# Kernel tuning notes

Measured on AMD Instinct MI355X. Metric: run time of the kernel, lower is better.

Reference implementation:

```python
import jax, jax.numpy as jnp
import numpy as np

B, L, D_MODEL = 4, 2048, 1024
N_HEADS, FEAT, HEAD_DIM = 16, 16, 64
CHUNK = 128
EPS = 1e-12


def taylor_exp(x):
    """2nd-order Taylor feature map of exp(q.k/sqrt(d)).
    x: (b, h, l, f) -> (b, h, l, 1 + f + f*f)"""
    f = x.shape[-1]
    r2 = jnp.sqrt(jnp.asarray(2.0, x.dtype))
    rd = jnp.sqrt(jnp.asarray(float(f), x.dtype))      # sqrt(d)
    rrd = jnp.sqrt(rd)                                  # d**0.25
    x2 = (x[..., :, None] * x[..., None, :]).reshape(*x.shape[:-1], f * f) / r2
    ones = jnp.ones_like(x[..., :1])
    return jnp.concatenate([ones, x / rrd, x2 / rd], axis=-1)


def setup_inputs() -> dict:
    key = jax.random.key(0)
    k1, k2, k3, k4, k5 = jax.random.split(key, 5)
    s = 0.02
    return {
        "hidden_states": jax.random.normal(k1, (B, L, D_MODEL), jnp.float32),
        "Wq": jax.random.normal(k2, (N_HEADS * FEAT, D_MODEL), jnp.float32) * s,
        "Wk": jax.random.normal(k3, (N_HEADS * FEAT, D_MODEL), jnp.float32) * s,
        "Wv": jax.random.normal(k4, (N_HEADS * HEAD_DIM, D_MODEL), jnp.float32) * s,
        "Wo": jax.random.normal(k5, (D_MODEL, N_HEADS * HEAD_DIM), jnp.float32) * s,
    }


def reference(hidden_states, Wq, Wk, Wv, Wo):
    b, l, _ = hidden_states.shape
    # projections (Linear without bias: x @ W.T)
    q = (hidden_states @ Wq.T).reshape(b, l, N_HEADS, FEAT).transpose(0, 2, 1, 3)
    k = (hidden_states @ Wk.T).reshape(b, l, N_HEADS, FEAT).transpose(0, 2, 1, 3)
    v = (hidden_states @ Wv.T).reshape(b, l, N_HEADS, HEAD_DIM).transpose(0, 2, 1, 3)

    qf = taylor_exp(q)  # (b, h, l, De) with De = 1 + f + f^2 = 273
    kf = taylor_exp(k)
    De = qf.shape[-1]

    # chunked causal linear attention: same math as cumulative kv-state
    n = l // CHUNK
    qc = jnp.moveaxis(qf.reshape(b, N_HEADS, n, CHUNK, De), 2, 0)       # (n,b,h,c,De)
    kc = jnp.moveaxis(kf.reshape(b, N_HEADS, n, CHUNK, De), 2, 0)
    vc = jnp.moveaxis(v.reshape(b, N_HEADS, n, CHUNK, HEAD_DIM), 2, 0)
    mask = jnp.tril(jnp.ones((CHUNK, CHUNK), qf.dtype))

    def step(carry, xs):
        S, z = carry                       # S: (b,h,De,e), z: (b,h,De)
        qi, ki, vi = xs
        attn = jnp.einsum('bhid,bhjd->bhij', qi, ki) * mask
        num = jnp.einsum('bhij,bhje->bhie', attn, vi) \
            + jnp.einsum('bhid,bhde->bhie', qi, S)
        den = attn.sum(-1) + jnp.einsum('bhid,bhd->bhi', qi, z)
        yi = num / (den[..., None] + EPS)
        S = S + jnp.einsum('bhjd,bhje->bhde', ki, vi)
        z = z + ki.sum(2)
        return (S, z), yi

    S0 = jnp.zeros((b, N_HEADS, De, HEAD_DIM), qf.dtype)
    z0 = jnp.zeros((b, N_HEADS, De), qf.dtype)
    _, ys = jax.lax.scan(step, (S0, z0), (qc, kc, vc))
    y = jnp.moveaxis(ys, 0, 2).reshape(b, N_HEADS, l, HEAD_DIM)          # (b,h,l,e)
    y = y.transpose(0, 2, 1, 3).reshape(b, l, N_HEADS * HEAD_DIM)        # (b,l,h*e)
    return y @ Wo.T
```

## Files before the change

kernel.cpp:

```cpp
#include <hip/hip_runtime.h>
#include <hip/hip_bf16.h>

#define BB 4
#define LL 2048
#define DM 1024
#define NH 16
#define FEAT 16
#define HD 64
#define CHUNK 128
#define NCHUNK 16
#define NEXT 80
#define SROW 23040
#define EPS 1e-12f
#define INV_R2RD 0.17677669529663688f
#define QKVLD 1536

typedef short bf16x8_t __attribute__((ext_vector_type(8)));
typedef float f32x4_t  __attribute__((ext_vector_type(4)));

__device__ __forceinline__ float b2f(unsigned short u) {
    union { unsigned int i; float f; } x; x.i = ((unsigned int)u) << 16; return x.f;
}
__device__ __forceinline__ unsigned short f2b(float f) {
    __hip_bfloat16 h = __float2bfloat16(f);
    return *reinterpret_cast<unsigned short*>(&h);
}

__global__ __launch_bounds__(256)
void cast_all(const float* __restrict__ hs, const float* __restrict__ wq,
              const float* __restrict__ wk, const float* __restrict__ wv,
              const float* __restrict__ wo, unsigned short* __restrict__ hs_bf,
              unsigned short* __restrict__ wqkv, unsigned short* __restrict__ wo_bf)
{
    const int i = (blockIdx.x * 256 + threadIdx.x) * 4;
    const float* s; unsigned short* d;
    if (i < 8388608)       { s = hs + i;             d = hs_bf + i; }
    else if (i < 8650752)  { s = wq + (i - 8388608); d = wqkv + (i - 8388608); }
    else if (i < 8912896)  { s = wk + (i - 8650752); d = wqkv + 262144 + (i - 8650752); }
    else if (i < 9961472)  { s = wv + (i - 8912896); d = wqkv + 524288 + (i - 8912896); }
    else if (i < 11010048) { s = wo + (i - 9961472); d = wo_bf + (i - 9961472); }
    else return;
    float4 v = *(const float4*)s;
    ushort4 o; o.x = f2b(v.x); o.y = f2b(v.y); o.z = f2b(v.z); o.w = f2b(v.w);
    *(ushort4*)d = o;
}

template <typename OutT>
__global__ __launch_bounds__(256)
void gemm_bf16(const unsigned short* __restrict__ A, const unsigned short* __restrict__ Bw,
               OutT* __restrict__ C, int M, int N, int K, int lda, int ldb, int ldc)
{
    __shared__ unsigned short As[128 * 32];
    __shared__ unsigned short Bs[128 * 32];
    const int tid  = threadIdx.x;
    const int wave = tid >> 6, lane = tid & 63;
    const int m0 = blockIdx.y * 128, n0 = blockIdx.x * 128;
    const int wm = (wave >> 1) * 64, wn = (wave & 1) * 64;
    const int srow = tid >> 2;
    const int skc  = tid & 3;
    const int ml = lane & 15, qq = lane >> 4;

    f32x4_t acc[4][4];
#pragma unroll
    for (int i = 0; i < 4; ++i)
#pragma unroll
        for (int j = 0; j < 4; ++j) acc[i][j] = (f32x4_t){0.f, 0.f, 0.f, 0.f};

    for (int k0 = 0; k0 < K; k0 += 32) {
#pragma unroll
        for (int p = 0; p < 2; ++p) {
            const int row = p * 64 + srow;
            const unsigned short* ga = A  + (size_t)(m0 + row) * lda + k0 + skc * 8;
            const unsigned short* gb = Bw + (size_t)(n0 + row) * ldb + k0 + skc * 8;
            unsigned short* la = As + (size_t)(p * 64 + wave * 16) * 32;
            unsigned short* lb = Bs + (size_t)(p * 64 + wave * 16) * 32;
            __builtin_amdgcn_global_load_lds((const __attribute__((address_space(1))) void*)ga,
                                             (__attribute__((address_space(3))) void*)la, 16, 0, 0);
            __builtin_amdgcn_global_load_lds((const __attribute__((address_space(1))) void*)gb,
                                             (__attribute__((address_space(3))) void*)lb, 16, 0, 0);
        }
        __syncthreads();
        bf16x8_t af[4], bfr[4];
#pragma unroll
        for (int i = 0; i < 4; ++i) {
            af[i]  = *(const bf16x8_t*)(As + (wm + i * 16 + ml) * 32 + qq * 8);
            bfr[i] = *(const bf16x8_t*)(Bs + (wn + i * 16 + ml) * 32 + qq * 8);
        }
#pragma unroll
        for (int i = 0; i < 4; ++i)
#pragma unroll
            for (int j = 0; j < 4; ++j)
                acc[i][j] = __builtin_amdgcn_mfma_f32_16x16x32_bf16(af[i], bfr[j], acc[i][j], 0, 0, 0);
        __syncthreads();
    }
#pragma unroll
    for (int i = 0; i < 4; ++i) {
        const int rbase = m0 + wm + i * 16 + qq * 4;
#pragma unroll
        for (int j = 0; j < 4; ++j) {
            const int col = n0 + wn + j * 16 + ml;
#pragma unroll
            for (int r = 0; r < 4; ++r) {
                const float v = acc[i][j][r];
                if constexpr (sizeof(OutT) == 2) {
                    ((unsigned short*)C)[(size_t)(rbase + r) * ldc + col] = f2b(v);
                } else {
                    ((float*)C)[(size_t)(rbase + r) * ldc + col] = v;
                }
            }
        }
    }
}

__global__ __launch_bounds__(256)
void state_kernel(const unsigned short* __restrict__ qkv, unsigned short* __restrict__ STg)
{
    __shared__ unsigned short KT[16 * 136];
    __shared__ unsigned short VT[80 * 136];

    const int x = blockIdx.x;
    const int c = x & 15, bh = x >> 4;
    const int b = bh >> 4, h = bh & 15;
    const int tid = threadIdx.x;
    const int wave = tid >> 6, lane = tid & 63;
    const int ml = lane & 15, kg8 = (lane >> 4) * 8;
    const size_t rowbase = (size_t)(b * LL + c * CHUNK);
    const size_t Sbase = (size_t)x * SROW;

    {
        const int row = tid >> 1, half = tid & 1;
        uint4 kv = *(const uint4*)(qkv + (rowbase + row) * QKVLD + 256 + h * 16 + half * 8);
        const unsigned short* kp = (const unsigned short*)&kv;
#pragma unroll
        for (int i = 0; i < 8; ++i) KT[(half * 8 + i) * 136 + row] = kp[i];
#pragma unroll
        for (int cc = 0; cc < 4; ++cc) {
            uint4 vv = *(const uint4*)(qkv + (rowbase + row) * QKVLD + 512 + h * 64 + half * 32 + cc * 8);
            const unsigned short* vp = (const unsigned short*)&vv;
#pragma unroll
            for (int i = 0; i < 8; ++i) VT[(half * 32 + cc * 8 + i) * 136 + row] = vp[i];
        }
        if (half == 0) {
            VT[64 * 136 + row] = 0x3F80;
        } else {
#pragma unroll
            for (int e = 65; e < 80; ++e) VT[e * 136 + row] = 0;
        }
    }
    __syncthreads();

    bf16x8_t bfr[5][4];
#pragma unroll
    for (int nt = 0; nt < 5; ++nt)
#pragma unroll
        for (int ks = 0; ks < 4; ++ks)
            bfr[nt][ks] = *(const bf16x8_t*)&VT[(nt * 16 + ml) * 136 + ks * 32 + kg8];

    for (int mt = wave; mt < 18; mt += 4) {
        const int d = mt * 16 + ml;
        bf16x8_t af[4];
#pragma unroll
        for (int ks = 0; ks < 4; ++ks) {
            const int jb = ks * 32 + kg8;
            unsigned short o[8];
            if (d >= 24 && d < 280) {
                const int e = d - 24, a = e >> 4, bq = e & 15;
                bf16x8_t ka = *(const bf16x8_t*)&KT[a  * 136 + jb];
                bf16x8_t kb = *(const bf16x8_t*)&KT[bq * 136 + jb];
#pragma unroll
                for (int j = 0; j < 8; ++j)
                    o[j] = f2b(b2f((unsigned short)ka[j]) * b2f((unsigned short)kb[j]) * INV_R2RD);
            } else if (d == 0) {
#pragma unroll
                for (int j = 0; j < 8; ++j) o[j] = 0x3F80;
            } else if (d <= 16) {
                bf16x8_t kx = *(const bf16x8_t*)&KT[(d - 1) * 136 + jb];
#pragma unroll
                for (int j = 0; j < 8; ++j) o[j] = f2b(b2f((unsigned short)kx[j]) * 0.5f);
            } else {
#pragma unroll
                for (int j = 0; j < 8; ++j) o[j] = 0;
            }
            af[ks] = *(const bf16x8_t*)o;
        }
        f32x4_t acc[5];
#pragma unroll
        for (int nt = 0; nt < 5; ++nt) acc[nt] = (f32x4_t){0.f, 0.f, 0.f, 0.f};
#pragma unroll
        for (int nt = 0; nt < 5; ++nt)
#pragma unroll
            for (int ks = 0; ks < 4; ++ks)
                acc[nt] = __builtin_amdgcn_mfma_f32_16x16x32_bf16(af[ks], bfr[nt][ks], acc[nt], 0, 0, 0);
#pragma unroll
        for (int nt = 0; nt < 5; ++nt) {
            ushort4 pk;
            pk.x = f2b(acc[nt][0]); pk.y = f2b(acc[nt][1]);
            pk.z = f2b(acc[nt][2]); pk.w = f2b(acc[nt][3]);
            *(ushort4*)(STg + Sbase + (size_t)mt * 1280 + (nt * 16 + ml) * 16 + (lane >> 4) * 4) = pk;
        }
    }
}

__global__ __launch_bounds__(256)
void scan_S(unsigned short* __restrict__ STg) {
    const int bh  = blockIdx.y;
    const int idx = blockIdx.x * 256 + threadIdx.x;
    if (idx >= SROW / 8) return;
    const size_t base = (size_t)bh * NCHUNK * SROW + (size_t)idx * 8;
    float acc[8] = {};
    for (int c = 0; c < NCHUNK; ++c) {
        unsigned short* p = STg + base + (size_t)c * SROW;
        uint4 v = *(const uint4*)p;
        const unsigned short* vp = (const unsigned short*)&v;
        uint4 o;
        unsigned short* op = (unsigned short*)&o;
#pragma unroll
        for (int i = 0; i < 8; ++i) { op[i] = f2b(acc[i]); acc[i] += b2f(vp[i]); }
        *(uint4*)p = o;
    }
}

#define OFF_VT 0
#define OFF_QP 0
#define OFF_KP 5120
#define OFF_A  10880
#define OFF_QS 28288

__global__ __launch_bounds__(256)
void out_kernel(const unsigned short* __restrict__ qkv_ro, const unsigned short* __restrict__ STg,
                unsigned short* __restrict__ qkv_w)
{
    __shared__ unsigned short smem[30336];

    const int x = blockIdx.x;
    const int c = x & 15, bh = x >> 4;
    const int b = bh >> 4, h = bh & 15;
    const int tid = threadIdx.x;
    const int w = tid >> 6, lane = tid & 63;
    const int ml = lane & 15, quad = lane >> 4, kg8 = quad * 8;
    const size_t rowbase = (size_t)(b * LL + c * CHUNK);
    const size_t Sbase = (size_t)x * SROW;

    const unsigned short* stp = STg + Sbase + (size_t)(quad >> 1) * 1280 + (quad & 1) * 8;
    bf16x8_t stf[2][5];
#pragma unroll
    for (int nt = 0; nt < 5; ++nt)
        stf[0][nt] = *(const bf16x8_t*)(stp + (nt * 16 + ml) * 16);

    {
        const int row = tid >> 1, half = tid & 1;
        uint4 qv = *(const uint4*)(qkv_ro + (rowbase + row) * QKVLD + h * 16 + half * 8);
        *(uint4*)&smem[OFF_QP + row * 40 + half * 8] = qv;
        *(uint4*)&smem[OFF_QP + row * 40 + 16 + half * 8] = (uint4){0, 0, 0, 0};
        *(uint4*)&smem[OFF_QS + row * 16 + half * 8] = qv;
        uint4 kv = *(const uint4*)(qkv_ro + (rowbase + row) * QKVLD + 256 + h * 16 + half * 8);
        *(uint4*)&smem[OFF_KP + row * 40 + half * 8] = kv;
        *(uint4*)&smem[OFF_KP + row * 40 + 16 + half * 8] = (uint4){0, 0, 0, 0};
    }
    __syncthreads();

    {
        bf16x8_t q0 = *(const bf16x8_t*)&smem[OFF_QP + (w * 32 + ml) * 40 + kg8];
        bf16x8_t q1 = *(const bf16x8_t*)&smem[OFF_QP + (w * 32 + 16 + ml) * 40 + kg8];
#pragma unroll
        for (int nt = 0; nt < 8; ++nt) {
            bf16x8_t kf = *(const bf16x8_t*)&smem[OFF_KP + (nt * 16 + ml) * 40 + kg8];
            f32x4_t a0 = __builtin_amdgcn_mfma_f32_16x16x32_bf16(q0, kf, (f32x4_t){0,0,0,0}, 0, 0, 0);
            f32x4_t a1 = __builtin_amdgcn_mfma_f32_16x16x32_bf16(q1, kf, (f32x4_t){0,0,0,0}, 0, 0, 0);
            const int j = nt * 16 + ml;
#pragma unroll
            for (int r = 0; r < 4; ++r) {
                int i0 = w * 32 + quad * 4 + r;
                float s0 = a0[r] * 0.25f;
                float v0 = (j <= i0) ? (1.f + s0 + 0.5f * s0 * s0) : 0.f;
                smem[OFF_A + i0 * 136 + j] = f2b(v0);
                int i1 = i0 + 16;
                float s1 = a1[r] * 0.25f;
                float v1 = (j <= i1) ? (1.f + s1 + 0.5f * s1 * s1) : 0.f;
                smem[OFF_A + i1 * 136 + j] = f2b(v1);
            }
        }
    }
    const int r0 = w * 32 + ml, r1 = r0 + 16;
    float qA[16], qB[16];
    {
        bf16x8_t t0 = *(const bf16x8_t*)&smem[OFF_QS + r0 * 16];
        bf16x8_t t1 = *(const bf16x8_t*)&smem[OFF_QS + r0 * 16 + 8];
        bf16x8_t t2 = *(const bf16x8_t*)&smem[OFF_QS + r1 * 16];
        bf16x8_t t3 = *(const bf16x8_t*)&smem[OFF_QS + r1 * 16 + 8];
#pragma unroll
        for (int i = 0; i < 8; ++i) {
            qA[i] = b2f((unsigned short)t0[i]); qA[8 + i] = b2f((unsigned short)t1[i]);
            qB[i] = b2f((unsigned short)t2[i]); qB[8 + i] = b2f((unsigned short)t3[i]);
        }
    }
    __syncthreads();

    {
        const int row = tid >> 1, half = tid & 1;
#pragma unroll
        for (int cc = 0; cc < 4; ++cc) {
            uint4 vv = *(const uint4*)(qkv_ro + (rowbase + row) * QKVLD + 512 + h * 64 + half * 32 + cc * 8);
            const unsigned short* vp = (const unsigned short*)&vv;
#pragma unroll
            for (int i = 0; i < 8; ++i) smem[OFF_VT + (half * 32 + cc * 8 + i) * 136 + row] = vp[i];
        }
        if (half == 0) {
            smem[OFF_VT + 64 * 136 + row] = 0x3F80;
        } else {
#pragma unroll
            for (int e = 65; e < 80; ++e) smem[OFF_VT + e * 136 + row] = 0;
        }
    }
    __syncthreads();

    f32x4_t acc[2][5];
#pragma unroll
    for (int mt = 0; mt < 2; ++mt)
#pragma unroll
        for (int nt = 0; nt < 5; ++nt) acc[mt][nt] = (f32x4_t){0.f, 0.f, 0.f, 0.f};

#pragma unroll
    for (int ks = 0; ks < 4; ++ks) {
        bf16x8_t af0 = *(const bf16x8_t*)&smem[OFF_A + (w * 32 + ml) * 136 + ks * 32 + kg8];
        bf16x8_t af1 = *(const bf16x8_t*)&smem[OFF_A + (w * 32 + 16 + ml) * 136 + ks * 32 + kg8];
#pragma unroll
        for (int nt = 0; nt < 5; ++nt) {
            bf16x8_t bv = *(const bf16x8_t*)&smem[OFF_VT + (nt * 16 + ml) * 136 + ks * 32 + kg8];
            acc[0][nt] = __builtin_amdgcn_mfma_f32_16x16x32_bf16(af0, bv, acc[0][nt], 0, 0, 0);
            acc[1][nt] = __builtin_amdgcn_mfma_f32_16x16x32_bf16(af1, bv, acc[1][nt], 0, 0, 0);
        }
    }

#pragma unroll
    for (int kq = 0; kq < 9; ++kq) {
        if (kq < 8) {
#pragma unroll
            for (int nt = 0; nt < 5; ++nt)
                stf[(kq + 1) & 1][nt] =
                    *(const bf16x8_t*)(stp + (size_t)(kq + 1) * 2560 + (nt * 16 + ml) * 16);
        }
        bf16x8_t qf[2];
#pragma unroll
        for (int mt = 0; mt < 2; ++mt) {
            const float* q = (mt == 0) ? qA : qB;
            const int qsrow = (mt == 0) ? r0 : r1;
            const int d0 = kq * 32 + kg8;
            unsigned short o[8];
            if (d0 >= 24 && d0 < 280) {
                const int e0 = d0 - 24;
                const float qa = b2f(smem[OFF_QS + qsrow * 16 + (e0 >> 4)]) * INV_R2RD;
                if ((e0 & 15) == 0) {
#pragma unroll
                    for (int j = 0; j < 8; ++j) o[j] = f2b(qa * q[j]);
                } else {
#pragma unroll
                    for (int j = 0; j < 8; ++j) o[j] = f2b(qa * q[8 + j]);
                }
            } else if (d0 == 0) {
                o[0] = 0x3F80;
#pragma unroll
                for (int j = 1; j < 8; ++j) o[j] = f2b(q[j - 1] * 0.5f);
            } else if (d0 == 8) {
#pragma unroll
                for (int j = 0; j < 8; ++j) o[j] = f2b(q[7 + j] * 0.5f);
            } else if (d0 == 16) {
                o[0] = f2b(q[15] * 0.5f);
#pragma unroll
                for (int j = 1; j < 8; ++j) o[j] = 0;
            } else {
#pragma unroll
                for (int j = 0; j < 8; ++j) o[j] = 0;
            }
            qf[mt] = *(const bf16x8_t*)o;
        }
#pragma unroll
        for (int nt = 0; nt < 5; ++nt) {
            acc[0][nt] = __builtin_amdgcn_mfma_f32_16x16x32_bf16(qf[0], stf[kq & 1][nt], acc[0][nt], 0, 0, 0);
            acc[1][nt] = __builtin_amdgcn_mfma_f32_16x16x32_bf16(qf[1], stf[kq & 1][nt], acc[1][nt], 0, 0, 0);
        }
    }

#pragma unroll
    for (int mt = 0; mt < 2; ++mt) {
        float den[4];
#pragma unroll
        for (int r = 0; r < 4; ++r) den[r] = __shfl(acc[mt][4][r], lane & 48);
#pragma unroll
        for (int r = 0; r < 4; ++r) {
            const size_t grow = rowbase + w * 32 + mt * 16 + quad * 4 + r;
            const float rc = 1.f / (den[r] + EPS);
#pragma unroll
            for (int nt = 0; nt < 4; ++nt)
                qkv_w[grow * QKVLD + 512 + h * 64 + nt * 16 + ml] = f2b(acc[mt][nt][r] * rc);
        }
    }
}

extern "C" void kernel_launch(void* const* d_in, const int* in_sizes, int n_in,
                              void* d_out, int out_size, void* d_ws, size_t ws_size,
                              hipStream_t stream)
{
    (void)in_sizes; (void)n_in; (void)out_size; (void)ws_size;
    const float* hs = (const float*)d_in[0];
    const float* Wq = (const float*)d_in[1];
    const float* Wk = (const float*)d_in[2];
    const float* Wv = (const float*)d_in[3];
    const float* Wo = (const float*)d_in[4];
    float* out = (float*)d_out;

    const int M = BB * LL;
    char* ws = (char*)d_ws;
    unsigned short* STg   = (unsigned short*)ws;
    unsigned short* hs_bf = (unsigned short*)ws;
    size_t off = 47185920;
    unsigned short* qkv   = (unsigned short*)(ws + off); off += 25165824;
    unsigned short* Wqkv  = (unsigned short*)(ws + off); off += 3145728;
    unsigned short* Wo_bf = (unsigned short*)(ws + off); off += 2097152;

    cast_all<<<10752, 256, 0, stream>>>(hs, Wq, Wk, Wv, Wo, hs_bf, Wqkv, Wo_bf);
    gemm_bf16<unsigned short><<<dim3(12, 64), 256, 0, stream>>>(hs_bf, Wqkv, qkv,
                                                                M, 1536, DM, DM, DM, QKVLD);
    state_kernel<<<1024, 256, 0, stream>>>(qkv, STg);
    scan_S<<<dim3(12, 64), 256, 0, stream>>>(STg);
    out_kernel<<<1024, 256, 0, stream>>>(qkv, STg, qkv);
    gemm_bf16<float><<<dim3(8, 64), 256, 0, stream>>>(qkv + 512, Wo_bf, out,
                                                      M, DM, DM, QKVLD, DM, DM);
}
```

Before: 216.9 us.

## Replace GEMM with 256x256-tile, 8-wave, double-buffered phased pipeline kernel

Replaces the simple 128x128 single-buffered bf16 GEMM, used for both the QKV and output projections, with a 256x256-tile, 512-thread kernel. It uses double-buffered XOR-swizzled LDS, K-step 64, and four interleaved phases that overlap global-to-LDS prefetch with MFMA work, plus setprio hints. The goal is to hide load latency, raise data reuse per tile and avoid LDS bank conflicts. The trade-offs are fewer blocks (192 and 128), which may underfill the 256 CUs, and heavy register and LDS use (128 KB).

```diff
diff --git a/kernel.cpp b/kernel.cpp
--- a/kernel.cpp
+++ b/kernel.cpp
@@ -46,62 +46,155 @@
 }
 
 template <typename OutT>
-__global__ __launch_bounds__(256)
-void gemm_bf16(const unsigned short* __restrict__ A, const unsigned short* __restrict__ Bw,
-               OutT* __restrict__ C, int M, int N, int K, int lda, int ldb, int ldc)
+__global__ __launch_bounds__(512, 2)
+void gemm_bf16_8ph(const unsigned short* __restrict__ A, const unsigned short* __restrict__ Bw,
+                   OutT* __restrict__ C, int K, int lda, int ldb, int ldc)
 {
-    __shared__ unsigned short As[128 * 32];
-    __shared__ unsigned short Bs[128 * 32];
+    __shared__ unsigned short lds[65536];
     const int tid  = threadIdx.x;
-    const int wave = tid >> 6, lane = tid & 63;
-    const int m0 = blockIdx.y * 128, n0 = blockIdx.x * 128;
-    const int wm = (wave >> 1) * 64, wn = (wave & 1) * 64;
-    const int srow = tid >> 2;
-    const int skc  = tid & 3;
-    const int ml = lane & 15, qq = lane >> 4;
-
-    f32x4_t acc[4][4];
-#pragma unroll
-    for (int i = 0; i < 4; ++i)
+    const int wid  = tid >> 6, lane = tid & 63;
+    const int wm   = wid >> 2, wn = wid & 3;
+    const int ml   = lane & 15, quad = lane >> 4;
+    const int m0   = blockIdx.y * 256, n0 = blockIdx.x * 256;
+    const int NT   = K >> 6;
+
+    const int srow  = tid >> 3;
+    const int scol  = ((tid & 7) ^ (srow & 7)) << 3;
+    const int wbase = wid << 9;
+
+    auto stage_half = [&](int t, int isB, int h) {
+        const unsigned short* g0 = isB ? Bw : A;
+        const int ld = isB ? ldb : lda;
+        const int rb = (isB ? n0 : m0) + h * 128 + srow;
+        const int k0 = t << 6;
+        unsigned short* lb = lds + (isB ? 32768 : 0) + ((t & 1) << 14) + (h << 13) + wbase;
+#pragma unroll
+        for (int l = 0; l < 2; ++l) {
+            const unsigned short* g = g0 + (size_t)(rb + l * 64) * ld + k0 + scol;
+            __builtin_amdgcn_global_load_lds((const __attribute__((address_space(1))) void*)g,
+                                             (__attribute__((address_space(3))) void*)(lb + l * 4096),
+                                             16, 0, 0);
+        }
+    };
+
+    f32x4_t acc[8][4];
+#pragma unroll
+    for (int i = 0; i < 8; ++i)
 #pragma unroll
         for (int j = 0; j < 4; ++j) acc[i][j] = (f32x4_t){0.f, 0.f, 0.f, 0.f};
 
-    for (int k0 = 0; k0 < K; k0 += 32) {
-#pragma unroll
-        for (int p = 0; p < 2; ++p) {
-            const int row = p * 64 + srow;
-            const unsigned short* ga = A  + (size_t)(m0 + row) * lda + k0 + skc * 8;
-            const unsigned short* gb = Bw + (size_t)(n0 + row) * ldb + k0 + skc * 8;
-            unsigned short* la = As + (size_t)(p * 64 + wave * 16) * 32;
-            unsigned short* lb = Bs + (size_t)(p * 64 + wave * 16) * 32;
-            __builtin_amdgcn_global_load_lds((const __attribute__((address_space(1))) void*)ga,
-                                             (__attribute__((address_space(3))) void*)la, 16, 0, 0);
-            __builtin_amdgcn_global_load_lds((const __attribute__((address_space(1))) void*)gb,
-                                             (__attribute__((address_space(3))) void*)lb, 16, 0, 0);
-        }
-        __syncthreads();
-        bf16x8_t af[4], bfr[4];
-#pragma unroll
-        for (int i = 0; i < 4; ++i) {
-            af[i]  = *(const bf16x8_t*)(As + (wm + i * 16 + ml) * 32 + qq * 8);
-            bfr[i] = *(const bf16x8_t*)(Bs + (wn + i * 16 + ml) * 32 + qq * 8);
-        }
-#pragma unroll
-        for (int i = 0; i < 4; ++i)
-#pragma unroll
-            for (int j = 0; j < 4; ++j)
-                acc[i][j] = __builtin_amdgcn_mfma_f32_16x16x32_bf16(af[i], bfr[j], acc[i][j], 0, 0, 0);
-        __syncthreads();
-    }
-#pragma unroll
-    for (int i = 0; i < 4; ++i) {
-        const int rbase = m0 + wm + i * 16 + qq * 4;
-#pragma unroll
-        for (int j = 0; j < 4; ++j) {
-            const int col = n0 + wn + j * 16 + ml;
+    stage_half(0, 0, 0); stage_half(0, 1, 0); stage_half(0, 0, 1); stage_half(0, 1, 1);
+    stage_half(1, 0, 0); stage_half(1, 1, 0); stage_half(1, 0, 1);
+    asm volatile("s_waitcnt vmcnt(6)" ::: "memory");
+    __builtin_amdgcn_s_barrier();
+
+    const int swz  = (ml & 7) << 3;
+    const int c0   = (quad << 3) ^ swz;
+    const int c1   = (32 + (quad << 3)) ^ swz;
+    const int arow = ml << 6;
+
+    bf16x8_t aA[4][2], bLo[2][2], bHi[2][2];
+
+    for (int t = 0; t < NT; ++t) {
+        const int ab = (t & 1) << 14;
+        const int bb = 32768 + ((t & 1) << 14);
+
+#pragma unroll
+        for (int m = 0; m < 4; ++m) {
+            const int r = ab + ((2 * m + wm) << 10) + arow;
+            aA[m][0] = *(const bf16x8_t*)&lds[r + c0];
+            aA[m][1] = *(const bf16x8_t*)&lds[r + c1];
+        }
+#pragma unroll
+        for (int n = 0; n < 2; ++n) {
+            const int r = bb + ((4 * n + wn) << 10) + arow;
+            bLo[n][0] = *(const bf16x8_t*)&lds[r + c0];
+            bLo[n][1] = *(const bf16x8_t*)&lds[r + c1];
+        }
+        if (t + 1 < NT) stage_half(t + 1, 1, 1);
+        __builtin_amdgcn_s_barrier();
+        asm volatile("s_waitcnt lgkmcnt(0)" ::: "memory");
+        __builtin_amdgcn_sched_barrier(0);
+        __builtin_amdgcn_s_setprio(1);
+#pragma unroll
+        for (int m = 0; m < 4; ++m)
+#pragma unroll
+            for (int n = 0; n < 2; ++n) {
+                acc[m][n] = __builtin_amdgcn_mfma_f32_16x16x32_bf16(aA[m][0], bLo[n][0], acc[m][n], 0, 0, 0);
+                acc[m][n] = __builtin_amdgcn_mfma_f32_16x16x32_bf16(aA[m][1], bLo[n][1], acc[m][n], 0, 0, 0);
+            }
+        __builtin_amdgcn_s_setprio(0);
+        __builtin_amdgcn_s_barrier();
+
+#pragma unroll
+        for (int n = 0; n < 2; ++n) {
+            const int r = bb + ((4 * (n + 2) + wn) << 10) + arow;
+            bHi[n][0] = *(const bf16x8_t*)&lds[r + c0];
+            bHi[n][1] = *(const bf16x8_t*)&lds[r + c1];
+        }
+        if (t + 2 < NT) stage_half(t + 2, 0, 0);
+        __builtin_amdgcn_s_barrier();
+        asm volatile("s_waitcnt lgkmcnt(0)" ::: "memory");
+        __builtin_amdgcn_sched_barrier(0);
+        __builtin_amdgcn_s_setprio(1);
+#pragma unroll
+        for (int m = 0; m < 4; ++m)
+#pragma unroll
+            for (int n = 0; n < 2; ++n) {
+                acc[m][2 + n] = __builtin_amdgcn_mfma_f32_16x16x32_bf16(aA[m][0], bHi[n][0], acc[m][2 + n], 0, 0, 0);
+                acc[m][2 + n] = __builtin_amdgcn_mfma_f32_16x16x32_bf16(aA[m][1], bHi[n][1], acc[m][2 + n], 0, 0, 0);
+            }
+        __builtin_amdgcn_s_setprio(0);
+        __builtin_amdgcn_s_barrier();
+
+#pragma unroll
+        for (int m = 0; m < 4; ++m) {
+            const int r = ab + ((2 * (m + 4) + wm) << 10) + arow;
+            aA[m][0] = *(const bf16x8_t*)&lds[r + c0];
+            aA[m][1] = *(const bf16x8_t*)&lds[r + c1];
+        }
+        if (t + 2 < NT) stage_half(t + 2, 1, 0);
+        __builtin_amdgcn_s_barrier();
+        asm volatile("s_waitcnt lgkmcnt(0)" ::: "memory");
+        __builtin_amdgcn_sched_barrier(0);
+        __builtin_amdgcn_s_setprio(1);
+#pragma unroll
+        for (int m = 0; m < 4; ++m)
+#pragma unroll
+            for (int n = 0; n < 2; ++n) {
+                acc[4 + m][2 + n] = __builtin_amdgcn_mfma_f32_16x16x32_bf16(aA[m][0], bHi[n][0], acc[4 + m][2 + n], 0, 0, 0);
+                acc[4 + m][2 + n] = __builtin_amdgcn_mfma_f32_16x16x32_bf16(aA[m][1], bHi[n][1], acc[4 + m][2 + n], 0, 0, 0);
+            }
+        __builtin_amdgcn_s_setprio(0);
+        __builtin_amdgcn_s_barrier();
+
+        if (t + 2 < NT) stage_half(t + 2, 0, 1);
+        __builtin_amdgcn_s_barrier();
+        asm volatile("s_waitcnt lgkmcnt(0)" ::: "memory");
+        __builtin_amdgcn_sched_barrier(0);
+        __builtin_amdgcn_s_setprio(1);
+#pragma unroll
+        for (int m = 0; m < 4; ++m)
+#pragma unroll
+            for (int n = 0; n < 2; ++n) {
+                acc[4 + m][n] = __builtin_amdgcn_mfma_f32_16x16x32_bf16(aA[m][0], bLo[n][0], acc[4 + m][n], 0, 0, 0);
+                acc[4 + m][n] = __builtin_amdgcn_mfma_f32_16x16x32_bf16(aA[m][1], bLo[n][1], acc[4 + m][n], 0, 0, 0);
+            }
+        __builtin_amdgcn_s_setprio(0);
+        if (t + 2 < NT)      asm volatile("s_waitcnt vmcnt(6)" ::: "memory");
+        else if (t + 1 < NT) asm volatile("s_waitcnt vmcnt(0)" ::: "memory");
+        __builtin_amdgcn_s_barrier();
+    }
+
+#pragma unroll
+    for (int m = 0; m < 8; ++m) {
+        const int rbase = m0 + (2 * m + wm) * 16 + quad * 4;
+#pragma unroll
+        for (int n = 0; n < 4; ++n) {
+            const int col = n0 + (4 * n + wn) * 16 + ml;
 #pragma unroll
             for (int r = 0; r < 4; ++r) {
-                const float v = acc[i][j][r];
+                const float v = acc[m][n][r];
                 if constexpr (sizeof(OutT) == 2) {
                     ((unsigned short*)C)[(size_t)(rbase + r) * ldc + col] = f2b(v);
                 } else {
@@ -409,7 +502,6 @@
     const float* Wo = (const float*)d_in[4];
     float* out = (float*)d_out;
 
-    const int M = BB * LL;
     char* ws = (char*)d_ws;
     unsigned short* STg   = (unsigned short*)ws;
     unsigned short* hs_bf = (unsigned short*)ws;
@@ -419,11 +511,11 @@
     unsigned short* Wo_bf = (unsigned short*)(ws + off); off += 2097152;
 
     cast_all<<<10752, 256, 0, stream>>>(hs, Wq, Wk, Wv, Wo, hs_bf, Wqkv, Wo_bf);
-    gemm_bf16<unsigned short><<<dim3(12, 64), 256, 0, stream>>>(hs_bf, Wqkv, qkv,
-                                                                M, 1536, DM, DM, DM, QKVLD);
+    gemm_bf16_8ph<unsigned short><<<dim3(6, 32), 512, 0, stream>>>(hs_bf, Wqkv, qkv,
+                                                                   DM, DM, DM, QKVLD);
     state_kernel<<<1024, 256, 0, stream>>>(qkv, STg);
     scan_S<<<dim3(12, 64), 256, 0, stream>>>(STg);
     out_kernel<<<1024, 256, 0, stream>>>(qkv, STg, qkv);
-    gemm_bf16<float><<<dim3(8, 64), 256, 0, stream>>>(qkv + 512, Wo_bf, out,
-                                                      M, DM, DM, QKVLD, DM, DM);
-}
+    gemm_bf16_8ph<float><<<dim3(4, 32), 512, 0, stream>>>(qkv + 512, Wo_bf, out,
+                                                          DM, QKVLD, DM, DM);
+}
```

Result: no change. 213.0 us (-1.8%).
